# Optimization experiments

Measured on AMD Instinct MI355X. Metric: run time of the kernel, lower is better.

## Reference

```python
import jax, jax.numpy as jnp
import numpy as np

N, E, IN, H, OUT = 100000, 600000, 128, 128, 64
BN_EPS = 1e-5


def setup_inputs() -> dict:
    key = jax.random.key(0)
    ks = jax.random.split(key, 8)
    def lin(k, i, o):
        return jax.random.normal(k, (i, o), jnp.float32) / np.float32(np.sqrt(i))
    return {
        "x": jax.random.normal(ks[0], (N, IN), jnp.float32),
        "edge_index": jax.random.randint(ks[1], (2, E), 0, N, dtype=jnp.int64),
        "W1": lin(ks[2], IN, H), "b1": jnp.zeros((H,), jnp.float32),
        "gamma": jnp.ones((H,), jnp.float32), "beta": jnp.zeros((H,), jnp.float32),
        "W2": lin(ks[3], H, H), "b2": jnp.zeros((H,), jnp.float32),
        "Wm1": lin(ks[4], H, H), "bm1": jnp.zeros((H,), jnp.float32),
        "Wm2": lin(ks[5], H, OUT), "bm2": jnp.zeros((OUT,), jnp.float32),
    }


def reference(x, edge_index, W1, b1, gamma, beta, W2, b2, Wm1, bm1, Wm2, bm2):
    # GINConv: h = MLP((1 + eps) * x + sum_{j in N(i)} x_j), eps = 0 (train_eps=False)
    src = edge_index[0]
    dst = edge_index[1]  # PyG aggregates messages at edge_index[1]
    agg = jax.ops.segment_sum(x[src], dst, num_segments=x.shape[0])  # [N, IN]
    h = agg + x
    # inner MLP: Linear -> BatchNorm (batch stats) -> ReLU -> Linear
    h = h @ W1 + b1
    mean = jnp.mean(h, axis=0)
    var = jnp.var(h, axis=0)
    h = (h - mean) * jax.lax.rsqrt(var + BN_EPS) * gamma + beta
    h = jax.nn.relu(h)
    h = h @ W2 + b2
    h = jax.nn.relu(h)  # .relu() after conv
    # output MLP (norm=None, dropout=0.5 -> identity at inference): Linear -> ReLU -> Linear
    h = jax.nn.relu(h @ Wm1 + bm1)
    return h @ Wm2 + bm2
```

## Files before the change

kernel.cpp:

```cpp
#include <hip/hip_runtime.h>
#include <hip/hip_bf16.h>
#include <stdint.h>

#define NNODES 100000
#define NEDGES 600000
#define SCAN_CHUNK 1024
#define SCAN_NB 98

typedef __attribute__((ext_vector_type(8))) short bf16x8;
typedef __attribute__((ext_vector_type(4))) float f32x4;

__device__ inline float b2f(short b) {
    union { unsigned u; float f; } v;
    v.u = ((unsigned)(unsigned short)b) << 16;
    return v.f;
}
__device__ inline short f2b(float f) {
    union { float f; unsigned u; } v;
    v.f = f;
    unsigned r = (v.u + 0x7FFFu + ((v.u >> 16) & 1u)) >> 16;
    return (short)r;
}
__device__ inline int swz(int row, int kbyte) {
    return (row * 256 + kbyte) ^ ((row & 7) << 4);
}
#define MFMA16(a, b, c) __builtin_amdgcn_mfma_f32_16x16x32_bf16(a, b, c, 0, 0, 0)

__global__ __launch_bounds__(256) void k_prep(const float* __restrict__ x,
                                              const float* __restrict__ W1,
                                              const float* __restrict__ W2,
                                              const float* __restrict__ Wm1,
                                              const float* __restrict__ Wm2,
                                              short* __restrict__ xb, short* __restrict__ Wt,
                                              int* __restrict__ pos, float* __restrict__ stats) {
    int i = blockIdx.x * 256 + threadIdx.x;
    if (i < (NNODES + 1) * 16) {
        bf16x8 o = (bf16x8){0, 0, 0, 0, 0, 0, 0, 0};
        if (i < NNODES * 16) {
            const float4* p = (const float4*)(x + (size_t)i * 8);
            float4 a = p[0], b = p[1];
            o[0] = f2b(a.x); o[1] = f2b(a.y); o[2] = f2b(a.z); o[3] = f2b(a.w);
            o[4] = f2b(b.x); o[5] = f2b(b.y); o[6] = f2b(b.z); o[7] = f2b(b.w);
        }
        *(bf16x8*)(xb + (size_t)i * 8) = o;
    }
    if (i < NNODES) pos[i] = 0;
    if (i < 57344) {
        float v;
        int c, k, base, ncb;
        if (i < 16384) {
            c = i >> 7; k = i & 127; v = W1[k * 128 + c]; base = 0; ncb = 8;
        } else if (i < 32768) {
            int j = i - 16384; c = j >> 7; k = j & 127; v = W2[k * 128 + c]; base = 16384; ncb = 8;
        } else if (i < 49152) {
            int j = i - 32768; c = j >> 7; k = j & 127; v = Wm1[k * 128 + c]; base = 32768; ncb = 8;
        } else {
            int j = i - 49152; c = j >> 7; k = j & 127; v = Wm2[k * 64 + c]; base = 49152; ncb = 4;
        }
        int kb = k >> 5, hi = (k >> 3) & 3, jj = k & 7;
        int cb = c >> 4, lr = c & 15;
        int lane = hi * 16 + lr;
        int dst = base + (((kb * ncb) + cb) * 64 + lane) * 8 + jj;
        Wt[dst] = f2b(v);
    }
    if (i < 256) stats[i] = 0.0f;
}


__global__ __launch_bounds__(256) void k_hist(const int* __restrict__ ei, int* __restrict__ cnt) {
    int e = blockIdx.x * 256 + threadIdx.x;
    if (e < NEDGES) atomicAdd(&cnt[ei[NEDGES + e]], 1);
}

__global__ __launch_bounds__(256) void k_scan1(const int* __restrict__ cnt, int* __restrict__ bsums) {
    __shared__ int sd[256];
    int b = blockIdx.x, t = threadIdx.x;
    int base = b * SCAN_CHUNK + t * 4;
    int s = 0;
#pragma unroll
    for (int i = 0; i < 4; ++i) {
        int idx = base + i;
        if (idx < NNODES) s += cnt[idx];
    }
    sd[t] = s;
    __syncthreads();
    for (int off = 128; off > 0; off >>= 1) {
        if (t < off) sd[t] += sd[t + off];
        __syncthreads();
    }
    if (t == 0) bsums[b] = sd[0];
}

__global__ __launch_bounds__(64) void k_scan2(int* __restrict__ bsums, int* __restrict__ rowptr) {
    if (threadIdx.x == 0 && blockIdx.x == 0) {
        int run = 0;
        for (int b = 0; b < SCAN_NB; ++b) {
            int v = bsums[b];
            bsums[b] = run;
            run += v;
        }
        rowptr[NNODES] = run;
    }
}

__global__ __launch_bounds__(256) void k_scan3(const int* __restrict__ cnt,
                                               const int* __restrict__ bsums,
                                               int* __restrict__ rowptr, int* __restrict__ pos) {
    __shared__ int sd[256];
    int b = blockIdx.x, t = threadIdx.x;
    int base = b * SCAN_CHUNK + t * 4;
    int v[4];
    int s = 0;
#pragma unroll
    for (int i = 0; i < 4; ++i) {
        int idx = base + i;
        v[i] = (idx < NNODES) ? cnt[idx] : 0;
        s += v[i];
    }
    sd[t] = s;
    __syncthreads();
    for (int off = 1; off < 256; off <<= 1) {
        int val = (t >= off) ? sd[t - off] : 0;
        __syncthreads();
        sd[t] += val;
        __syncthreads();
    }
    int run = sd[t] - s + bsums[b];
#pragma unroll
    for (int i = 0; i < 4; ++i) {
        int idx = base + i;
        if (idx < NNODES) {
            rowptr[idx] = run;
            pos[idx] = run;
            run += v[i];
        }
    }
}

__global__ __launch_bounds__(256) void k_fill(const int* __restrict__ ei, int* __restrict__ pos,
                                              int* __restrict__ elist) {
    int e = blockIdx.x * 256 + threadIdx.x;
    if (e >= NEDGES) return;
    int src = ei[e];
    int dst = ei[NEDGES + e];
    int p = atomicAdd(&pos[dst], 1);
    elist[p] = src;
}

__global__ __launch_bounds__(256) void k_agg(const short* __restrict__ xb,
                                             const int* __restrict__ rowptr,
                                             const int* __restrict__ elist,
                                             short* __restrict__ bufb) {
    int t = threadIdx.x;
    int w = t >> 6, lane = t & 63;
    int node = blockIdx.x * 4 + w;
    if (node >= NNODES) return;
    int beg = rowptr[node];
    int end = rowptr[node + 1];
    int deg = end - beg;
    int total = deg + 1;
    int sub = lane & 31, half = lane >> 5;
    const uint2* xr = (const uint2*)xb;

    float acc0 = 0.f, acc1 = 0.f, acc2 = 0.f, acc3 = 0.f;

    for (int base = 0; base < total; base += 64) {
        int j = base + lane;
        int ej = NNODES;
        if (j < total) ej = (j == 0) ? node : elist[beg + j - 1];
        int cnt = min(64, total - base);
        int pairs = (cnt + 1) >> 1;
        for (int i = 0; i < pairs; i += 4) {
            int j0 = 2 * i + half;
            int r0 = __shfl(ej, j0);
            int r1 = __shfl(ej, j0 + 2);
            int r2 = __shfl(ej, j0 + 4);
            int r3 = __shfl(ej, j0 + 6);
            uint2 v0 = xr[(size_t)r0 * 32 + sub];
            uint2 v1 = xr[(size_t)r1 * 32 + sub];
            uint2 v2 = xr[(size_t)r2 * 32 + sub];
            uint2 v3 = xr[(size_t)r3 * 32 + sub];
            acc0 += b2f((short)(v0.x & 0xFFFF)) + b2f((short)(v1.x & 0xFFFF)) +
                    b2f((short)(v2.x & 0xFFFF)) + b2f((short)(v3.x & 0xFFFF));
            acc1 += b2f((short)(v0.x >> 16)) + b2f((short)(v1.x >> 16)) +
                    b2f((short)(v2.x >> 16)) + b2f((short)(v3.x >> 16));
            acc2 += b2f((short)(v0.y & 0xFFFF)) + b2f((short)(v1.y & 0xFFFF)) +
                    b2f((short)(v2.y & 0xFFFF)) + b2f((short)(v3.y & 0xFFFF));
            acc3 += b2f((short)(v0.y >> 16)) + b2f((short)(v1.y >> 16)) +
                    b2f((short)(v2.y >> 16)) + b2f((short)(v3.y >> 16));
        }
    }
    acc0 += __shfl_xor(acc0, 32);
    acc1 += __shfl_xor(acc1, 32);
    acc2 += __shfl_xor(acc2, 32);
    acc3 += __shfl_xor(acc3, 32);
    if (half == 0) {
        uint2 o;
        o.x = ((uint32_t)(unsigned short)f2b(acc1) << 16) | (uint32_t)(unsigned short)f2b(acc0);
        o.y = ((uint32_t)(unsigned short)f2b(acc3) << 16) | (uint32_t)(unsigned short)f2b(acc2);
        ((uint2*)bufb)[(size_t)node * 32 + sub] = o;
    }
}

__global__ __launch_bounds__(256) void k_stats(const short* __restrict__ bufb,
                                               const short* __restrict__ W1pk,
                                               float* __restrict__ stats) {
    __shared__ float Sred[2][4][128];
    int t = threadIdx.x, w = t >> 6, l = t & 63;
    int r0 = blockIdx.x * 128;
    int row0 = (w & 1) * 64, col0 = (w >> 1) * 64;

    f32x4 acc[4][4];
#pragma unroll
    for (int r = 0; r < 4; ++r)
#pragma unroll
        for (int c = 0; c < 4; ++c) acc[r][c] = (f32x4){0.f, 0.f, 0.f, 0.f};

#pragma unroll
    for (int kb = 0; kb < 4; ++kb) {
        bf16x8 af[4], bw[4];
#pragma unroll
        for (int r = 0; r < 4; ++r)
            af[r] = *(const bf16x8*)(bufb + (size_t)(r0 + row0 + r * 16 + (l & 15)) * 128 +
                                     kb * 32 + (l >> 4) * 8);
#pragma unroll
        for (int c = 0; c < 4; ++c)
            bw[c] = *(const bf16x8*)(W1pk + ((kb * 8 + (w >> 1) * 4 + c) * 64 + l) * 8);
#pragma unroll
        for (int r = 0; r < 4; ++r)
#pragma unroll
            for (int c = 0; c < 4; ++c) acc[r][c] = MFMA16(af[r], bw[c], acc[r][c]);
    }

    float s[4], q[4];
#pragma unroll
    for (int c = 0; c < 4; ++c) { s[c] = 0.f; q[c] = 0.f; }
#pragma unroll
    for (int c = 0; c < 4; ++c)
#pragma unroll
        for (int r = 0; r < 4; ++r)
#pragma unroll
            for (int rr = 0; rr < 4; ++rr) {
                int grow = r0 + row0 + r * 16 + (l >> 4) * 4 + rr;
                if (grow < NNODES) {
                    float v = acc[r][c][rr];
                    s[c] += v;
                    q[c] += v * v;
                }
            }
#pragma unroll
    for (int c = 0; c < 4; ++c) {
        s[c] += __shfl_xor(s[c], 16); s[c] += __shfl_xor(s[c], 32);
        q[c] += __shfl_xor(q[c], 16); q[c] += __shfl_xor(q[c], 32);
    }
    if (l < 16) {
#pragma unroll
        for (int c = 0; c < 4; ++c) {
            Sred[0][w][col0 + c * 16 + l] = s[c];
            Sred[1][w][col0 + c * 16 + l] = q[c];
        }
    }
    __syncthreads();
    if (t < 128) {
        int wb = (t < 64) ? 0 : 2;
        atomicAdd(stats + t, Sred[0][wb][t] + Sred[0][wb + 1][t]);
        atomicAdd(stats + 128 + t, Sred[1][wb][t] + Sred[1][wb + 1][t]);
    }
}

__global__ __launch_bounds__(256) void k_mlp(const short* __restrict__ bufb,
                                             const float* __restrict__ stats,
                                             const float* __restrict__ gamma,
                                             const float* __restrict__ beta,
                                             const short* __restrict__ Wt,
                                             const float* __restrict__ b2,
                                             const float* __restrict__ bm1,
                                             const float* __restrict__ bm2,
                                             float* __restrict__ out) {
    __shared__ __align__(16) short act[128 * 128];
    __shared__ float scale[128], shift[128];

    int t = threadIdx.x, w = t >> 6, l = t & 63;
    int r0 = blockIdx.x * 128;
    const short* W1pk = Wt;
    const short* W2pk = Wt + 16384;
    const short* Wm1pk = Wt + 32768;
    const short* Wm2pk = Wt + 49152;

    if (t < 128) {
        float mean = stats[t] * (1.0f / NNODES);
        float var = stats[128 + t] * (1.0f / NNODES) - mean * mean;
        var = fmaxf(var, 0.0f);
        float inv = rsqrtf(var + 1e-5f);
        float sc = gamma[t] * inv;
        scale[t] = sc;
        shift[t] = beta[t] - mean * sc;
    }
    __syncthreads();

    int row0 = (w & 1) * 64, col0 = (w >> 1) * 64;
    f32x4 acc[4][4];

#pragma unroll
    for (int r = 0; r < 4; ++r)
#pragma unroll
        for (int c = 0; c < 4; ++c) acc[r][c] = (f32x4){0.f, 0.f, 0.f, 0.f};
#pragma unroll
    for (int kb = 0; kb < 4; ++kb) {
        bf16x8 af[4], bw[4];
#pragma unroll
        for (int r = 0; r < 4; ++r)
            af[r] = *(const bf16x8*)(bufb + (size_t)(r0 + row0 + r * 16 + (l & 15)) * 128 +
                                     kb * 32 + (l >> 4) * 8);
#pragma unroll
        for (int c = 0; c < 4; ++c)
            bw[c] = *(const bf16x8*)(W1pk + ((kb * 8 + (w >> 1) * 4 + c) * 64 + l) * 8);
#pragma unroll
        for (int r = 0; r < 4; ++r)
#pragma unroll
            for (int c = 0; c < 4; ++c) acc[r][c] = MFMA16(af[r], bw[c], acc[r][c]);
    }
#pragma unroll
    for (int c = 0; c < 4; ++c) {
        int col = col0 + c * 16 + (l & 15);
        float sc_ = scale[col], sh_ = shift[col];
#pragma unroll
        for (int r = 0; r < 4; ++r)
#pragma unroll
            for (int rr = 0; rr < 4; ++rr) {
                int row = row0 + r * 16 + (l >> 4) * 4 + rr;
                *(short*)((char*)act + swz(row, col * 2)) =
                    f2b(fmaxf(acc[r][c][rr] * sc_ + sh_, 0.f));
            }
    }
    __syncthreads();

#pragma unroll
    for (int r = 0; r < 4; ++r)
#pragma unroll
        for (int c = 0; c < 4; ++c) acc[r][c] = (f32x4){0.f, 0.f, 0.f, 0.f};
#pragma unroll
    for (int kb = 0; kb < 4; ++kb) {
        int kbyte = kb * 64 + (l >> 4) * 16;
        bf16x8 af[4], bw[4];
#pragma unroll
        for (int r = 0; r < 4; ++r)
            af[r] = *(const bf16x8*)((char*)act + swz(row0 + r * 16 + (l & 15), kbyte));
#pragma unroll
        for (int c = 0; c < 4; ++c)
            bw[c] = *(const bf16x8*)(W2pk + ((kb * 8 + (w >> 1) * 4 + c) * 64 + l) * 8);
#pragma unroll
        for (int r = 0; r < 4; ++r)
#pragma unroll
            for (int c = 0; c < 4; ++c) acc[r][c] = MFMA16(af[r], bw[c], acc[r][c]);
    }
    __syncthreads();
#pragma unroll
    for (int c = 0; c < 4; ++c) {
        int col = col0 + c * 16 + (l & 15);
        float bias = b2[col];
#pragma unroll
        for (int r = 0; r < 4; ++r)
#pragma unroll
            for (int rr = 0; rr < 4; ++rr) {
                int row = row0 + r * 16 + (l >> 4) * 4 + rr;
                *(short*)((char*)act + swz(row, col * 2)) = f2b(fmaxf(acc[r][c][rr] + bias, 0.f));
            }
    }
    __syncthreads();

#pragma unroll
    for (int r = 0; r < 4; ++r)
#pragma unroll
        for (int c = 0; c < 4; ++c) acc[r][c] = (f32x4){0.f, 0.f, 0.f, 0.f};
#pragma unroll
    for (int kb = 0; kb < 4; ++kb) {
        int kbyte = kb * 64 + (l >> 4) * 16;
        bf16x8 af[4], bw[4];
#pragma unroll
        for (int r = 0; r < 4; ++r)
            af[r] = *(const bf16x8*)((char*)act + swz(row0 + r * 16 + (l & 15), kbyte));
#pragma unroll
        for (int c = 0; c < 4; ++c)
            bw[c] = *(const bf16x8*)(Wm1pk + ((kb * 8 + (w >> 1) * 4 + c) * 64 + l) * 8);
#pragma unroll
        for (int r = 0; r < 4; ++r)
#pragma unroll
            for (int c = 0; c < 4; ++c) acc[r][c] = MFMA16(af[r], bw[c], acc[r][c]);
    }
    __syncthreads();
#pragma unroll
    for (int c = 0; c < 4; ++c) {
        int col = col0 + c * 16 + (l & 15);
        float bias = bm1[col];
#pragma unroll
        for (int r = 0; r < 4; ++r)
#pragma unroll
            for (int rr = 0; rr < 4; ++rr) {
                int row = row0 + r * 16 + (l >> 4) * 4 + rr;
                *(short*)((char*)act + swz(row, col * 2)) = f2b(fmaxf(acc[r][c][rr] + bias, 0.f));
            }
    }
    __syncthreads();

    int row0q = w * 32;
    f32x4 a2[2][4];
#pragma unroll
    for (int r = 0; r < 2; ++r)
#pragma unroll
        for (int c = 0; c < 4; ++c) a2[r][c] = (f32x4){0.f, 0.f, 0.f, 0.f};
#pragma unroll
    for (int kb = 0; kb < 4; ++kb) {
        int kbyte = kb * 64 + (l >> 4) * 16;
        bf16x8 af[2], bw[4];
#pragma unroll
        for (int r = 0; r < 2; ++r)
            af[r] = *(const bf16x8*)((char*)act + swz(row0q + r * 16 + (l & 15), kbyte));
#pragma unroll
        for (int c = 0; c < 4; ++c)
            bw[c] = *(const bf16x8*)(Wm2pk + ((kb * 4 + c) * 64 + l) * 8);
#pragma unroll
        for (int r = 0; r < 2; ++r)
#pragma unroll
            for (int c = 0; c < 4; ++c) a2[r][c] = MFMA16(af[r], bw[c], a2[r][c]);
    }
#pragma unroll
    for (int c = 0; c < 4; ++c) {
        float bias = bm2[c * 16 + (l & 15)];
#pragma unroll
        for (int r = 0; r < 2; ++r)
#pragma unroll
            for (int rr = 0; rr < 4; ++rr) {
                int grow = r0 + row0q + r * 16 + (l >> 4) * 4 + rr;
                if (grow < NNODES)
                    out[(size_t)grow * 64 + c * 16 + (l & 15)] = a2[r][c][rr] + bias;
            }
    }
}

extern "C" void kernel_launch(void* const* d_in, const int* in_sizes, int n_in,
                              void* d_out, int out_size, void* d_ws, size_t ws_size,
                              hipStream_t stream) {
    const float* x     = (const float*)d_in[0];
    const int*   ei    = (const int*)d_in[1];
    const float* W1    = (const float*)d_in[2];
    const float* gamma = (const float*)d_in[4];
    const float* beta  = (const float*)d_in[5];
    const float* W2    = (const float*)d_in[6];
    const float* b2    = (const float*)d_in[7];
    const float* Wm1   = (const float*)d_in[8];
    const float* bm1   = (const float*)d_in[9];
    const float* Wm2   = (const float*)d_in[10];
    const float* bm2   = (const float*)d_in[11];
    float* out = (float*)d_out;

    char* ws = (char*)d_ws;
    short* xb    = (short*)ws;
    short* bufb  = xb + (size_t)(NNODES + 1) * 128;
    short* Wt    = bufb + (size_t)(NNODES + 128) * 128;
    float* stats = (float*)(Wt + 57344);
    int* rowptr  = (int*)(stats + 256);
    int* pos     = rowptr + (NNODES + 1);
    int* elist   = pos + NNODES;
    int* bsums   = elist + NEDGES;

    int gE = (NEDGES + 255) / 256;
    int gPrep = ((NNODES + 1) * 16 + 255) / 256;

    k_prep<<<gPrep, 256, 0, stream>>>(x, W1, W2, Wm1, Wm2, xb, Wt, pos, stats);
    k_hist<<<gE, 256, 0, stream>>>(ei, pos);
    k_scan1<<<SCAN_NB, 256, 0, stream>>>(pos, bsums);
    k_scan2<<<1, 64, 0, stream>>>(bsums, rowptr);
    k_scan3<<<SCAN_NB, 256, 0, stream>>>(pos, bsums, rowptr, pos);
    k_fill<<<gE, 256, 0, stream>>>(ei, pos, elist);
    k_agg<<<(NNODES + 3) / 4, 256, 0, stream>>>(xb, rowptr, elist, bufb);

    int nblk = (NNODES + 127) / 128;
    k_stats<<<nblk, 256, 0, stream>>>(bufb, Wt, stats);
    k_mlp<<<nblk, 256, 0, stream>>>(bufb, stats, gamma, beta, Wt, b2, bm1, bm2, out);
}
```

Measured before the change: 180.1 us.

## Restructure MLP kernel to single-wave 64-row blocks without barriers

The fused MLP kernel now runs one 64-thread wave per 64-row tile instead of four waves per 128-row tile. Each wave computes all 128 output columns in two passes, so every __syncthreads between layers is gone. A-fragments for all K blocks are held in registers, and biases are staged in shared memory. The kernel also raises wave priority with s_setprio around the MFMA loops and cuts per-block LDS, which should allow more blocks per CU. In exchange, each block loads the weights twice as often relative to rows computed, and register pressure rises from holding 16 A fragments.

```diff
diff --git a/kernel.cpp b/kernel.cpp
--- a/kernel.cpp
+++ b/kernel.cpp
@@ -268,172 +268,198 @@
     }
 }
 
-__global__ __launch_bounds__(256) void k_mlp(const short* __restrict__ bufb,
-                                             const float* __restrict__ stats,
-                                             const float* __restrict__ gamma,
-                                             const float* __restrict__ beta,
-                                             const short* __restrict__ Wt,
-                                             const float* __restrict__ b2,
-                                             const float* __restrict__ bm1,
-                                             const float* __restrict__ bm2,
-                                             float* __restrict__ out) {
-    __shared__ __align__(16) short act[128 * 128];
-    __shared__ float scale[128], shift[128];
-
-    int t = threadIdx.x, w = t >> 6, l = t & 63;
-    int r0 = blockIdx.x * 128;
+__global__ __launch_bounds__(64) void k_mlp(const short* __restrict__ bufb,
+                                            const float* __restrict__ stats,
+                                            const float* __restrict__ gamma,
+                                            const float* __restrict__ beta,
+                                            const short* __restrict__ Wt,
+                                            const float* __restrict__ b2,
+                                            const float* __restrict__ bm1,
+                                            const float* __restrict__ bm2,
+                                            float* __restrict__ out) {
+    __shared__ __align__(16) short act[64 * 128];
+    __shared__ float scale[128], shift[128], b2s[128], bm1s[128], bm2s[64];
+
+    int l = threadIdx.x;
+    int lr = l & 15, hi = l >> 4;
+    size_t r0w = (size_t)blockIdx.x * 64;
     const short* W1pk = Wt;
     const short* W2pk = Wt + 16384;
     const short* Wm1pk = Wt + 32768;
     const short* Wm2pk = Wt + 49152;
 
-    if (t < 128) {
-        float mean = stats[t] * (1.0f / NNODES);
-        float var = stats[128 + t] * (1.0f / NNODES) - mean * mean;
+#pragma unroll
+    for (int i = 0; i < 2; ++i) {
+        int idx = l + i * 64;
+        float mean = stats[idx] * (1.0f / NNODES);
+        float var = stats[128 + idx] * (1.0f / NNODES) - mean * mean;
         var = fmaxf(var, 0.0f);
         float inv = rsqrtf(var + 1e-5f);
-        float sc = gamma[t] * inv;
-        scale[t] = sc;
-        shift[t] = beta[t] - mean * sc;
-    }
+        float sc = gamma[idx] * inv;
+        scale[idx] = sc;
+        shift[idx] = beta[idx] - mean * sc;
+        b2s[idx] = b2[idx];
+        bm1s[idx] = bm1[idx];
+    }
+    bm2s[l] = bm2[l];
     __syncthreads();
 
-    int row0 = (w & 1) * 64, col0 = (w >> 1) * 64;
+    bf16x8 af[4][4];
     f32x4 acc[4][4];
 
 #pragma unroll
+    for (int kb = 0; kb < 4; ++kb)
+#pragma unroll
+        for (int r = 0; r < 4; ++r)
+            af[kb][r] = *(const bf16x8*)(bufb + (r0w + r * 16 + lr) * 128 + kb * 32 + hi * 8);
+
+#pragma unroll
+    for (int p = 0; p < 2; ++p) {
+#pragma unroll
+        for (int r = 0; r < 4; ++r)
+#pragma unroll
+            for (int c = 0; c < 4; ++c) acc[r][c] = (f32x4){0.f, 0.f, 0.f, 0.f};
+        __builtin_amdgcn_s_setprio(1);
+#pragma unroll
+        for (int kb = 0; kb < 4; ++kb) {
+            bf16x8 bw[4];
+#pragma unroll
+            for (int c = 0; c < 4; ++c)
+                bw[c] = *(const bf16x8*)(W1pk + ((kb * 8 + p * 4 + c) * 64 + l) * 8);
+#pragma unroll
+            for (int r = 0; r < 4; ++r)
+#pragma unroll
+                for (int c = 0; c < 4; ++c) acc[r][c] = MFMA16(af[kb][r], bw[c], acc[r][c]);
+        }
+        __builtin_amdgcn_s_setprio(0);
+#pragma unroll
+        for (int c = 0; c < 4; ++c) {
+            int col = p * 64 + c * 16 + lr;
+            float sc_ = scale[col], sh_ = shift[col];
+#pragma unroll
+            for (int r = 0; r < 4; ++r)
+#pragma unroll
+                for (int rr = 0; rr < 4; ++rr) {
+                    int row = r * 16 + hi * 4 + rr;
+                    *(short*)((char*)act + swz(row, col * 2)) =
+                        f2b(fmaxf(acc[r][c][rr] * sc_ + sh_, 0.f));
+                }
+        }
+    }
+
+#pragma unroll
+    for (int kb = 0; kb < 4; ++kb)
+#pragma unroll
+        for (int r = 0; r < 4; ++r)
+            af[kb][r] = *(const bf16x8*)((char*)act + swz(r * 16 + lr, kb * 64 + hi * 16));
+
+#pragma unroll
+    for (int p = 0; p < 2; ++p) {
+#pragma unroll
+        for (int r = 0; r < 4; ++r)
+#pragma unroll
+            for (int c = 0; c < 4; ++c) acc[r][c] = (f32x4){0.f, 0.f, 0.f, 0.f};
+        __builtin_amdgcn_s_setprio(1);
+#pragma unroll
+        for (int kb = 0; kb < 4; ++kb) {
+            bf16x8 bw[4];
+#pragma unroll
+            for (int c = 0; c < 4; ++c)
+                bw[c] = *(const bf16x8*)(W2pk + ((kb * 8 + p * 4 + c) * 64 + l) * 8);
+#pragma unroll
+            for (int r = 0; r < 4; ++r)
+#pragma unroll
+                for (int c = 0; c < 4; ++c) acc[r][c] = MFMA16(af[kb][r], bw[c], acc[r][c]);
+        }
+        __builtin_amdgcn_s_setprio(0);
+#pragma unroll
+        for (int c = 0; c < 4; ++c) {
+            int col = p * 64 + c * 16 + lr;
+            float bias = b2s[col];
+#pragma unroll
+            for (int r = 0; r < 4; ++r)
+#pragma unroll
+                for (int rr = 0; rr < 4; ++rr) {
+                    int row = r * 16 + hi * 4 + rr;
+                    *(short*)((char*)act + swz(row, col * 2)) =
+                        f2b(fmaxf(acc[r][c][rr] + bias, 0.f));
+                }
+        }
+    }
+
+#pragma unroll
+    for (int kb = 0; kb < 4; ++kb)
+#pragma unroll
+        for (int r = 0; r < 4; ++r)
+            af[kb][r] = *(const bf16x8*)((char*)act + swz(r * 16 + lr, kb * 64 + hi * 16));
+
+#pragma unroll
+    for (int p = 0; p < 2; ++p) {
+#pragma unroll
+        for (int r = 0; r < 4; ++r)
+#pragma unroll
+            for (int c = 0; c < 4; ++c) acc[r][c] = (f32x4){0.f, 0.f, 0.f, 0.f};
+        __builtin_amdgcn_s_setprio(1);
+#pragma unroll
+        for (int kb = 0; kb < 4; ++kb) {
+            bf16x8 bw[4];
+#pragma unroll
+            for (int c = 0; c < 4; ++c)
+                bw[c] = *(const bf16x8*)(Wm1pk + ((kb * 8 + p * 4 + c) * 64 + l) * 8);
+#pragma unroll
+            for (int r = 0; r < 4; ++r)
+#pragma unroll
+                for (int c = 0; c < 4; ++c) acc[r][c] = MFMA16(af[kb][r], bw[c], acc[r][c]);
+        }
+        __builtin_amdgcn_s_setprio(0);
+#pragma unroll
+        for (int c = 0; c < 4; ++c) {
+            int col = p * 64 + c * 16 + lr;
+            float bias = bm1s[col];
+#pragma unroll
+            for (int r = 0; r < 4; ++r)
+#pragma unroll
+                for (int rr = 0; rr < 4; ++rr) {
+                    int row = r * 16 + hi * 4 + rr;
+                    *(short*)((char*)act + swz(row, col * 2)) =
+                        f2b(fmaxf(acc[r][c][rr] + bias, 0.f));
+                }
+        }
+    }
+
+#pragma unroll
+    for (int kb = 0; kb < 4; ++kb)
+#pragma unroll
+        for (int r = 0; r < 4; ++r)
+            af[kb][r] = *(const bf16x8*)((char*)act + swz(r * 16 + lr, kb * 64 + hi * 16));
+
+#pragma unroll
     for (int r = 0; r < 4; ++r)
 #pragma unroll
         for (int c = 0; c < 4; ++c) acc[r][c] = (f32x4){0.f, 0.f, 0.f, 0.f};
+    __builtin_amdgcn_s_setprio(1);
 #pragma unroll
     for (int kb = 0; kb < 4; ++kb) {
-        bf16x8 af[4], bw[4];
-#pragma unroll
-        for (int r = 0; r < 4; ++r)
-            af[r] = *(const bf16x8*)(bufb + (size_t)(r0 + row0 + r * 16 + (l & 15)) * 128 +
-                                     kb * 32 + (l >> 4) * 8);
-#pragma unroll
-        for (int c = 0; c < 4; ++c)
-            bw[c] = *(const bf16x8*)(W1pk + ((kb * 8 + (w >> 1) * 4 + c) * 64 + l) * 8);
-#pragma unroll
-        for (int r = 0; r < 4; ++r)
-#pragma unroll
-            for (int c = 0; c < 4; ++c) acc[r][c] = MFMA16(af[r], bw[c], acc[r][c]);
-    }
-#pragma unroll
-    for (int c = 0; c < 4; ++c) {
-        int col = col0 + c * 16 + (l & 15);
-        float sc_ = scale[col], sh_ = shift[col];
-#pragma unroll
-        for (int r = 0; r < 4; ++r)
-#pragma unroll
-            for (int rr = 0; rr < 4; ++rr) {
-                int row = row0 + r * 16 + (l >> 4) * 4 + rr;
-                *(short*)((char*)act + swz(row, col * 2)) =
-                    f2b(fmaxf(acc[r][c][rr] * sc_ + sh_, 0.f));
-            }
-    }
-    __syncthreads();
-
-#pragma unroll
-    for (int r = 0; r < 4; ++r)
-#pragma unroll
-        for (int c = 0; c < 4; ++c) acc[r][c] = (f32x4){0.f, 0.f, 0.f, 0.f};
-#pragma unroll
-    for (int kb = 0; kb < 4; ++kb) {
-        int kbyte = kb * 64 + (l >> 4) * 16;
-        bf16x8 af[4], bw[4];
-#pragma unroll
-        for (int r = 0; r < 4; ++r)
-            af[r] = *(const bf16x8*)((char*)act + swz(row0 + r * 16 + (l & 15), kbyte));
-#pragma unroll
-        for (int c = 0; c < 4; ++c)
-            bw[c] = *(const bf16x8*)(W2pk + ((kb * 8 + (w >> 1) * 4 + c) * 64 + l) * 8);
-#pragma unroll
-        for (int r = 0; r < 4; ++r)
-#pragma unroll
-            for (int c = 0; c < 4; ++c) acc[r][c] = MFMA16(af[r], bw[c], acc[r][c]);
-    }
-    __syncthreads();
-#pragma unroll
-    for (int c = 0; c < 4; ++c) {
-        int col = col0 + c * 16 + (l & 15);
-        float bias = b2[col];
-#pragma unroll
-        for (int r = 0; r < 4; ++r)
-#pragma unroll
-            for (int rr = 0; rr < 4; ++rr) {
-                int row = row0 + r * 16 + (l >> 4) * 4 + rr;
-                *(short*)((char*)act + swz(row, col * 2)) = f2b(fmaxf(acc[r][c][rr] + bias, 0.f));
-            }
-    }
-    __syncthreads();
-
-#pragma unroll
-    for (int r = 0; r < 4; ++r)
-#pragma unroll
-        for (int c = 0; c < 4; ++c) acc[r][c] = (f32x4){0.f, 0.f, 0.f, 0.f};
-#pragma unroll
-    for (int kb = 0; kb < 4; ++kb) {
-        int kbyte = kb * 64 + (l >> 4) * 16;
-        bf16x8 af[4], bw[4];
-#pragma unroll
-        for (int r = 0; r < 4; ++r)
-            af[r] = *(const bf16x8*)((char*)act + swz(row0 + r * 16 + (l & 15), kbyte));
-#pragma unroll
-        for (int c = 0; c < 4; ++c)
-            bw[c] = *(const bf16x8*)(Wm1pk + ((kb * 8 + (w >> 1) * 4 + c) * 64 + l) * 8);
-#pragma unroll
-        for (int r = 0; r < 4; ++r)
-#pragma unroll
-            for (int c = 0; c < 4; ++c) acc[r][c] = MFMA16(af[r], bw[c], acc[r][c]);
-    }
-    __syncthreads();
-#pragma unroll
-    for (int c = 0; c < 4; ++c) {
-        int col = col0 + c * 16 + (l & 15);
-        float bias = bm1[col];
-#pragma unroll
-        for (int r = 0; r < 4; ++r)
-#pragma unroll
-            for (int rr = 0; rr < 4; ++rr) {
-                int row = row0 + r * 16 + (l >> 4) * 4 + rr;
-                *(short*)((char*)act + swz(row, col * 2)) = f2b(fmaxf(acc[r][c][rr] + bias, 0.f));
-            }
-    }
-    __syncthreads();
-
-    int row0q = w * 32;
-    f32x4 a2[2][4];
-#pragma unroll
-    for (int r = 0; r < 2; ++r)
-#pragma unroll
-        for (int c = 0; c < 4; ++c) a2[r][c] = (f32x4){0.f, 0.f, 0.f, 0.f};
-#pragma unroll
-    for (int kb = 0; kb < 4; ++kb) {
-        int kbyte = kb * 64 + (l >> 4) * 16;
-        bf16x8 af[2], bw[4];
-#pragma unroll
-        for (int r = 0; r < 2; ++r)
-            af[r] = *(const bf16x8*)((char*)act + swz(row0q + r * 16 + (l & 15), kbyte));
+        bf16x8 bw[4];
 #pragma unroll
         for (int c = 0; c < 4; ++c)
             bw[c] = *(const bf16x8*)(Wm2pk + ((kb * 4 + c) * 64 + l) * 8);
 #pragma unroll
-        for (int r = 0; r < 2; ++r)
-#pragma unroll
-            for (int c = 0; c < 4; ++c) a2[r][c] = MFMA16(af[r], bw[c], a2[r][c]);
-    }
+        for (int r = 0; r < 4; ++r)
+#pragma unroll
+            for (int c = 0; c < 4; ++c) acc[r][c] = MFMA16(af[kb][r], bw[c], acc[r][c]);
+    }
+    __builtin_amdgcn_s_setprio(0);
 #pragma unroll
     for (int c = 0; c < 4; ++c) {
-        float bias = bm2[c * 16 + (l & 15)];
-#pragma unroll
-        for (int r = 0; r < 2; ++r)
+        float bias = bm2s[c * 16 + lr];
+#pragma unroll
+        for (int r = 0; r < 4; ++r)
 #pragma unroll
             for (int rr = 0; rr < 4; ++rr) {
-                int grow = r0 + row0q + r * 16 + (l >> 4) * 4 + rr;
+                size_t grow = r0w + r * 16 + hi * 4 + rr;
                 if (grow < NNODES)
-                    out[(size_t)grow * 64 + c * 16 + (l & 15)] = a2[r][c][rr] + bias;
+                    out[grow * 64 + c * 16 + lr] = acc[r][c][rr] + bias;
             }
     }
 }
@@ -475,7 +501,8 @@
     k_fill<<<gE, 256, 0, stream>>>(ei, pos, elist);
     k_agg<<<(NNODES + 3) / 4, 256, 0, stream>>>(xb, rowptr, elist, bufb);
 
-    int nblk = (NNODES + 127) / 128;
-    k_stats<<<nblk, 256, 0, stream>>>(bufb, Wt, stats);
-    k_mlp<<<nblk, 256, 0, stream>>>(bufb, stats, gamma, beta, Wt, b2, bm1, bm2, out);
-}
+    int nblkS = (NNODES + 127) / 128;
+    k_stats<<<nblkS, 256, 0, stream>>>(bufb, Wt, stats);
+    int nblkM = (NNODES + 63) / 64;
+    k_mlp<<<nblkM, 64, 0, stream>>>(bufb, stats, gamma, beta, Wt, b2, bm1, bm2, out);
+}
```

After: 183.5 us. Within noise of the previous version (+1.9%).

## Keep MLP chain in registers via transposed MFMA and shuffle redistribution; single-block scan

Applied to the files above, without the earlier changes.

The MLP kernel is restructured so each wave owns 16 nodes and computes transposed products (W^T·h), holding activations in registers. Between layers the outputs are repacked to bf16 and redistributed across lanes with shuffles, which removes the shared-memory activation tile and its barriers. Weights are repacked ct-major to match this access order, and launch bounds ask for higher occupancy. The three-kernel scan is replaced by a single 1024-thread block, which cuts launches but serialises the scan onto one CU with strided per-thread loops.

```diff
diff --git a/kernel.cpp b/kernel.cpp
--- a/kernel.cpp
+++ b/kernel.cpp
@@ -4,11 +4,10 @@
 
 #define NNODES 100000
 #define NEDGES 600000
-#define SCAN_CHUNK 1024
-#define SCAN_NB 98
 
 typedef __attribute__((ext_vector_type(8))) short bf16x8;
 typedef __attribute__((ext_vector_type(4))) float f32x4;
+typedef __attribute__((ext_vector_type(4))) unsigned int u32x4;
 
 __device__ inline float b2f(short b) {
     union { unsigned u; float f; } v;
@@ -21,8 +20,8 @@
     unsigned r = (v.u + 0x7FFFu + ((v.u >> 16) & 1u)) >> 16;
     return (short)r;
 }
-__device__ inline int swz(int row, int kbyte) {
-    return (row * 256 + kbyte) ^ ((row & 7) << 4);
+__device__ inline unsigned packbf(float lo, float hi) {
+    return ((unsigned)(unsigned short)f2b(hi) << 16) | (unsigned)(unsigned short)f2b(lo);
 }
 #define MFMA16(a, b, c) __builtin_amdgcn_mfma_f32_16x16x32_bf16(a, b, c, 0, 0, 0)
 
@@ -46,22 +45,21 @@
     }
     if (i < NNODES) pos[i] = 0;
     if (i < 57344) {
-        float v;
-        int c, k, base, ncb;
-        if (i < 16384) {
-            c = i >> 7; k = i & 127; v = W1[k * 128 + c]; base = 0; ncb = 8;
-        } else if (i < 32768) {
-            int j = i - 16384; c = j >> 7; k = j & 127; v = W2[k * 128 + c]; base = 16384; ncb = 8;
-        } else if (i < 49152) {
-            int j = i - 32768; c = j >> 7; k = j & 127; v = Wm1[k * 128 + c]; base = 32768; ncb = 8;
-        } else {
-            int j = i - 49152; c = j >> 7; k = j & 127; v = Wm2[k * 64 + c]; base = 49152; ncb = 4;
-        }
-        int kb = k >> 5, hi = (k >> 3) & 3, jj = k & 7;
-        int cb = c >> 4, lr = c & 15;
-        int lane = hi * 16 + lr;
-        int dst = base + (((kb * ncb) + cb) * 64 + lane) * 8 + jj;
-        Wt[dst] = f2b(v);
+        int jj, lane, kt, ct;
+        const float* W;
+        int ldw, off;
+        if (i < 16384) { off = i; W = W1; ldw = 128; }
+        else if (i < 32768) { off = i - 16384; W = W2; ldw = 128; }
+        else if (i < 49152) { off = i - 32768; W = Wm1; ldw = 128; }
+        else { off = i - 49152; W = Wm2; ldw = 64; }
+        jj = off & 7;
+        lane = (off >> 3) & 63;
+        kt = (off >> 9) & 3;
+        ct = (off >> 11) & 7;
+        int lr = lane & 15, hi = lane >> 4;
+        int c = ct * 16 + lr;
+        int k = kt * 32 + hi * 8 + jj;
+        Wt[i] = f2b(W[k * ldw + c]);
     }
     if (i < 256) stats[i] = 0.0f;
 }
@@ -72,69 +70,35 @@
     if (e < NEDGES) atomicAdd(&cnt[ei[NEDGES + e]], 1);
 }
 
-__global__ __launch_bounds__(256) void k_scan1(const int* __restrict__ cnt, int* __restrict__ bsums) {
-    __shared__ int sd[256];
-    int b = blockIdx.x, t = threadIdx.x;
-    int base = b * SCAN_CHUNK + t * 4;
+__global__ __launch_bounds__(1024) void k_scan(const int* __restrict__ cnt,
+                                               int* __restrict__ rowptr, int* __restrict__ pos) {
+    __shared__ int sd[1024];
+    int t = threadIdx.x;
+    int base = t * 98;
     int s = 0;
-#pragma unroll
-    for (int i = 0; i < 4; ++i) {
+    for (int i = 0; i < 98; ++i) {
         int idx = base + i;
         if (idx < NNODES) s += cnt[idx];
     }
     sd[t] = s;
     __syncthreads();
-    for (int off = 128; off > 0; off >>= 1) {
-        if (t < off) sd[t] += sd[t + off];
+    for (int off = 1; off < 1024; off <<= 1) {
+        int v = (t >= off) ? sd[t - off] : 0;
         __syncthreads();
-    }
-    if (t == 0) bsums[b] = sd[0];
-}
-
-__global__ __launch_bounds__(64) void k_scan2(int* __restrict__ bsums, int* __restrict__ rowptr) {
-    if (threadIdx.x == 0 && blockIdx.x == 0) {
-        int run = 0;
-        for (int b = 0; b < SCAN_NB; ++b) {
-            int v = bsums[b];
-            bsums[b] = run;
-            run += v;
-        }
-        rowptr[NNODES] = run;
-    }
-}
-
-__global__ __launch_bounds__(256) void k_scan3(const int* __restrict__ cnt,
-                                               const int* __restrict__ bsums,
-                                               int* __restrict__ rowptr, int* __restrict__ pos) {
-    __shared__ int sd[256];
-    int b = blockIdx.x, t = threadIdx.x;
-    int base = b * SCAN_CHUNK + t * 4;
-    int v[4];
-    int s = 0;
-#pragma unroll
-    for (int i = 0; i < 4; ++i) {
-        int idx = base + i;
-        v[i] = (idx < NNODES) ? cnt[idx] : 0;
-        s += v[i];
-    }
-    sd[t] = s;
-    __syncthreads();
-    for (int off = 1; off < 256; off <<= 1) {
-        int val = (t >= off) ? sd[t - off] : 0;
+        sd[t] += v;
         __syncthreads();
-        sd[t] += val;
-        __syncthreads();
-    }
-    int run = sd[t] - s + bsums[b];
-#pragma unroll
-    for (int i = 0; i < 4; ++i) {
+    }
+    int run = sd[t] - s;
+    for (int i = 0; i < 98; ++i) {
         int idx = base + i;
         if (idx < NNODES) {
+            int v = cnt[idx];
             rowptr[idx] = run;
             pos[idx] = run;
-            run += v[i];
-        }
-    }
+            run += v;
+        }
+    }
+    if (t == 1023) rowptr[NNODES] = run;
 }
 
 __global__ __launch_bounds__(256) void k_fill(const int* __restrict__ ei, int* __restrict__ pos,
@@ -225,7 +189,7 @@
                                      kb * 32 + (l >> 4) * 8);
 #pragma unroll
         for (int c = 0; c < 4; ++c)
-            bw[c] = *(const bf16x8*)(W1pk + ((kb * 8 + (w >> 1) * 4 + c) * 64 + l) * 8);
+            bw[c] = *(const bf16x8*)(W1pk + ((((w >> 1) * 4 + c) * 4 + kb) * 64 + l) * 8);
 #pragma unroll
         for (int r = 0; r < 4; ++r)
 #pragma unroll
@@ -268,20 +232,20 @@
     }
 }
 
-__global__ __launch_bounds__(256) void k_mlp(const short* __restrict__ bufb,
-                                             const float* __restrict__ stats,
-                                             const float* __restrict__ gamma,
-                                             const float* __restrict__ beta,
-                                             const short* __restrict__ Wt,
-                                             const float* __restrict__ b2,
-                                             const float* __restrict__ bm1,
-                                             const float* __restrict__ bm2,
-                                             float* __restrict__ out) {
-    __shared__ __align__(16) short act[128 * 128];
-    __shared__ float scale[128], shift[128];
+__global__ __launch_bounds__(256, 4) void k_mlp(const short* __restrict__ bufb,
+                                                const float* __restrict__ stats,
+                                                const float* __restrict__ gamma,
+                                                const float* __restrict__ beta,
+                                                const short* __restrict__ Wt,
+                                                const float* __restrict__ b2,
+                                                const float* __restrict__ bm1,
+                                                const float* __restrict__ bm2,
+                                                float* __restrict__ out) {
+    __shared__ float scale[128], shift[128], b2s[128], bm1s[128], bm2s[64];
 
     int t = threadIdx.x, w = t >> 6, l = t & 63;
-    int r0 = blockIdx.x * 128;
+    int lr = l & 15, hi = l >> 4;
+    size_t node0 = (size_t)blockIdx.x * 64 + w * 16;
     const short* W1pk = Wt;
     const short* W2pk = Wt + 16384;
     const short* Wm1pk = Wt + 32768;
@@ -295,146 +259,99 @@
         float sc = gamma[t] * inv;
         scale[t] = sc;
         shift[t] = beta[t] - mean * sc;
-    }
+        b2s[t] = b2[t];
+        bm1s[t] = bm1[t];
+    }
+    if (t < 64) bm2s[t] = bm2[t];
     __syncthreads();
 
-    int row0 = (w & 1) * 64, col0 = (w >> 1) * 64;
-    f32x4 acc[4][4];
-
-#pragma unroll
-    for (int r = 0; r < 4; ++r)
-#pragma unroll
-        for (int c = 0; c < 4; ++c) acc[r][c] = (f32x4){0.f, 0.f, 0.f, 0.f};
-#pragma unroll
-    for (int kb = 0; kb < 4; ++kb) {
-        bf16x8 af[4], bw[4];
-#pragma unroll
-        for (int r = 0; r < 4; ++r)
-            af[r] = *(const bf16x8*)(bufb + (size_t)(r0 + row0 + r * 16 + (l & 15)) * 128 +
-                                     kb * 32 + (l >> 4) * 8);
-#pragma unroll
-        for (int c = 0; c < 4; ++c)
-            bw[c] = *(const bf16x8*)(W1pk + ((kb * 8 + (w >> 1) * 4 + c) * 64 + l) * 8);
-#pragma unroll
-        for (int r = 0; r < 4; ++r)
-#pragma unroll
-            for (int c = 0; c < 4; ++c) acc[r][c] = MFMA16(af[r], bw[c], acc[r][c]);
-    }
-#pragma unroll
-    for (int c = 0; c < 4; ++c) {
-        int col = col0 + c * 16 + (l & 15);
-        float sc_ = scale[col], sh_ = shift[col];
-#pragma unroll
-        for (int r = 0; r < 4; ++r)
-#pragma unroll
-            for (int rr = 0; rr < 4; ++rr) {
-                int row = row0 + r * 16 + (l >> 4) * 4 + rr;
-                *(short*)((char*)act + swz(row, col * 2)) =
-                    f2b(fmaxf(acc[r][c][rr] * sc_ + sh_, 0.f));
-            }
-    }
-    __syncthreads();
-
-#pragma unroll
-    for (int r = 0; r < 4; ++r)
-#pragma unroll
-        for (int c = 0; c < 4; ++c) acc[r][c] = (f32x4){0.f, 0.f, 0.f, 0.f};
-#pragma unroll
-    for (int kb = 0; kb < 4; ++kb) {
-        int kbyte = kb * 64 + (l >> 4) * 16;
-        bf16x8 af[4], bw[4];
-#pragma unroll
-        for (int r = 0; r < 4; ++r)
-            af[r] = *(const bf16x8*)((char*)act + swz(row0 + r * 16 + (l & 15), kbyte));
-#pragma unroll
-        for (int c = 0; c < 4; ++c)
-            bw[c] = *(const bf16x8*)(W2pk + ((kb * 8 + (w >> 1) * 4 + c) * 64 + l) * 8);
-#pragma unroll
-        for (int r = 0; r < 4; ++r)
-#pragma unroll
-            for (int c = 0; c < 4; ++c) acc[r][c] = MFMA16(af[r], bw[c], acc[r][c]);
-    }
-    __syncthreads();
-#pragma unroll
-    for (int c = 0; c < 4; ++c) {
-        int col = col0 + c * 16 + (l & 15);
-        float bias = b2[col];
-#pragma unroll
-        for (int r = 0; r < 4; ++r)
-#pragma unroll
-            for (int rr = 0; rr < 4; ++rr) {
-                int row = row0 + r * 16 + (l >> 4) * 4 + rr;
-                *(short*)((char*)act + swz(row, col * 2)) = f2b(fmaxf(acc[r][c][rr] + bias, 0.f));
-            }
-    }
-    __syncthreads();
-
-#pragma unroll
-    for (int r = 0; r < 4; ++r)
-#pragma unroll
-        for (int c = 0; c < 4; ++c) acc[r][c] = (f32x4){0.f, 0.f, 0.f, 0.f};
-#pragma unroll
-    for (int kb = 0; kb < 4; ++kb) {
-        int kbyte = kb * 64 + (l >> 4) * 16;
-        bf16x8 af[4], bw[4];
-#pragma unroll
-        for (int r = 0; r < 4; ++r)
-            af[r] = *(const bf16x8*)((char*)act + swz(row0 + r * 16 + (l & 15), kbyte));
-#pragma unroll
-        for (int c = 0; c < 4; ++c)
-            bw[c] = *(const bf16x8*)(Wm1pk + ((kb * 8 + (w >> 1) * 4 + c) * 64 + l) * 8);
-#pragma unroll
-        for (int r = 0; r < 4; ++r)
-#pragma unroll
-            for (int c = 0; c < 4; ++c) acc[r][c] = MFMA16(af[r], bw[c], acc[r][c]);
-    }
-    __syncthreads();
-#pragma unroll
-    for (int c = 0; c < 4; ++c) {
-        int col = col0 + c * 16 + (l & 15);
-        float bias = bm1[col];
-#pragma unroll
-        for (int r = 0; r < 4; ++r)
-#pragma unroll
-            for (int rr = 0; rr < 4; ++rr) {
-                int row = row0 + r * 16 + (l >> 4) * 4 + rr;
-                *(short*)((char*)act + swz(row, col * 2)) = f2b(fmaxf(acc[r][c][rr] + bias, 0.f));
-            }
-    }
-    __syncthreads();
-
-    int row0q = w * 32;
-    f32x4 a2[2][4];
-#pragma unroll
-    for (int r = 0; r < 2; ++r)
-#pragma unroll
-        for (int c = 0; c < 4; ++c) a2[r][c] = (f32x4){0.f, 0.f, 0.f, 0.f};
-#pragma unroll
-    for (int kb = 0; kb < 4; ++kb) {
-        int kbyte = kb * 64 + (l >> 4) * 16;
-        bf16x8 af[2], bw[4];
-#pragma unroll
-        for (int r = 0; r < 2; ++r)
-            af[r] = *(const bf16x8*)((char*)act + swz(row0q + r * 16 + (l & 15), kbyte));
-#pragma unroll
-        for (int c = 0; c < 4; ++c)
-            bw[c] = *(const bf16x8*)(Wm2pk + ((kb * 4 + c) * 64 + l) * 8);
-#pragma unroll
-        for (int r = 0; r < 2; ++r)
-#pragma unroll
-            for (int c = 0; c < 4; ++c) a2[r][c] = MFMA16(af[r], bw[c], a2[r][c]);
-    }
-#pragma unroll
-    for (int c = 0; c < 4; ++c) {
-        float bias = bm2[c * 16 + (l & 15)];
-#pragma unroll
-        for (int r = 0; r < 2; ++r)
-#pragma unroll
-            for (int rr = 0; rr < 4; ++rr) {
-                int grow = r0 + row0q + r * 16 + (l >> 4) * 4 + rr;
-                if (grow < NNODES)
-                    out[(size_t)grow * 64 + c * 16 + (l & 15)] = a2[r][c][rr] + bias;
-            }
+    bf16x8 bv[4];
+#pragma unroll
+    for (int kt = 0; kt < 4; ++kt)
+        bv[kt] = *(const bf16x8*)(bufb + (node0 + lr) * 128 + kt * 32 + hi * 8);
+
+    unsigned pw[8][2];
+
+#pragma unroll
+    for (int ct = 0; ct < 8; ++ct) {
+        f32x4 a = (f32x4){0.f, 0.f, 0.f, 0.f};
+#pragma unroll
+        for (int kt = 0; kt < 4; ++kt)
+            a = MFMA16(*(const bf16x8*)(W1pk + ((ct * 4 + kt) * 64 + l) * 8), bv[kt], a);
+        int c0 = ct * 16 + hi * 4;
+        float4 sc4 = *(const float4*)&scale[c0];
+        float4 sh4 = *(const float4*)&shift[c0];
+        float v0 = fmaxf(a[0] * sc4.x + sh4.x, 0.f);
+        float v1 = fmaxf(a[1] * sc4.y + sh4.y, 0.f);
+        float v2 = fmaxf(a[2] * sc4.z + sh4.z, 0.f);
+        float v3 = fmaxf(a[3] * sc4.w + sh4.w, 0.f);
+        pw[ct][0] = packbf(v0, v1);
+        pw[ct][1] = packbf(v2, v3);
+    }
+
+#define REDIST()                                                                        \
+    {                                                                                   \
+        int h2 = hi >> 1, h1 = hi & 1;                                                  \
+        _Pragma("unroll") for (int kt = 0; kt < 4; ++kt) {                              \
+            unsigned nw[4];                                                             \
+            _Pragma("unroll") for (int jp = 0; jp < 4; ++jp) {                          \
+                int srcl = (2 * h1 + (jp >> 1)) * 16 + lr;                              \
+                unsigned ve = (unsigned)__shfl((int)pw[2 * kt][jp & 1], srcl);          \
+                unsigned vo = (unsigned)__shfl((int)pw[2 * kt + 1][jp & 1], srcl);      \
+                nw[jp] = h2 ? vo : ve;                                                  \
+            }                                                                           \
+            u32x4 uq = (u32x4){nw[0], nw[1], nw[2], nw[3]};                             \
+            bv[kt] = __builtin_bit_cast(bf16x8, uq);                                    \
+        }                                                                               \
+    }
+    REDIST();
+
+#pragma unroll
+    for (int ct = 0; ct < 8; ++ct) {
+        f32x4 a = (f32x4){0.f, 0.f, 0.f, 0.f};
+#pragma unroll
+        for (int kt = 0; kt < 4; ++kt)
+            a = MFMA16(*(const bf16x8*)(W2pk + ((ct * 4 + kt) * 64 + l) * 8), bv[kt], a);
+        int c0 = ct * 16 + hi * 4;
+        float4 bb = *(const float4*)&b2s[c0];
+        float v0 = fmaxf(a[0] + bb.x, 0.f);
+        float v1 = fmaxf(a[1] + bb.y, 0.f);
+        float v2 = fmaxf(a[2] + bb.z, 0.f);
+        float v3 = fmaxf(a[3] + bb.w, 0.f);
+        pw[ct][0] = packbf(v0, v1);
+        pw[ct][1] = packbf(v2, v3);
+    }
+    REDIST();
+
+#pragma unroll
+    for (int ct = 0; ct < 8; ++ct) {
+        f32x4 a = (f32x4){0.f, 0.f, 0.f, 0.f};
+#pragma unroll
+        for (int kt = 0; kt < 4; ++kt)
+            a = MFMA16(*(const bf16x8*)(Wm1pk + ((ct * 4 + kt) * 64 + l) * 8), bv[kt], a);
+        int c0 = ct * 16 + hi * 4;
+        float4 bb = *(const float4*)&bm1s[c0];
+        float v0 = fmaxf(a[0] + bb.x, 0.f);
+        float v1 = fmaxf(a[1] + bb.y, 0.f);
+        float v2 = fmaxf(a[2] + bb.z, 0.f);
+        float v3 = fmaxf(a[3] + bb.w, 0.f);
+        pw[ct][0] = packbf(v0, v1);
+        pw[ct][1] = packbf(v2, v3);
+    }
+    REDIST();
+
+#pragma unroll
+    for (int ct = 0; ct < 4; ++ct) {
+        f32x4 a = (f32x4){0.f, 0.f, 0.f, 0.f};
+#pragma unroll
+        for (int kt = 0; kt < 4; ++kt)
+            a = MFMA16(bv[kt], *(const bf16x8*)(Wm2pk + ((ct * 4 + kt) * 64 + l) * 8), a);
+        float bias = bm2s[ct * 16 + lr];
+#pragma unroll
+        for (int rr = 0; rr < 4; ++rr) {
+            size_t grow = node0 + hi * 4 + rr;
+            if (grow < NNODES) out[grow * 64 + ct * 16 + lr] = a[rr] + bias;
+        }
     }
 }
 
@@ -462,20 +379,18 @@
     int* rowptr  = (int*)(stats + 256);
     int* pos     = rowptr + (NNODES + 1);
     int* elist   = pos + NNODES;
-    int* bsums   = elist + NEDGES;
 
     int gE = (NEDGES + 255) / 256;
     int gPrep = ((NNODES + 1) * 16 + 255) / 256;
 
     k_prep<<<gPrep, 256, 0, stream>>>(x, W1, W2, Wm1, Wm2, xb, Wt, pos, stats);
     k_hist<<<gE, 256, 0, stream>>>(ei, pos);
-    k_scan1<<<SCAN_NB, 256, 0, stream>>>(pos, bsums);
-    k_scan2<<<1, 64, 0, stream>>>(bsums, rowptr);
-    k_scan3<<<SCAN_NB, 256, 0, stream>>>(pos, bsums, rowptr, pos);
+    k_scan<<<1, 1024, 0, stream>>>(pos, rowptr, pos);
     k_fill<<<gE, 256, 0, stream>>>(ei, pos, elist);
     k_agg<<<(NNODES + 3) / 4, 256, 0, stream>>>(xb, rowptr, elist, bufb);
 
-    int nblk = (NNODES + 127) / 128;
-    k_stats<<<nblk, 256, 0, stream>>>(bufb, Wt, stats);
-    k_mlp<<<nblk, 256, 0, stream>>>(bufb, stats, gamma, beta, Wt, b2, bm1, bm2, out);
-}
+    int nblkS = (NNODES + 127) / 128;
+    k_stats<<<nblkS, 256, 0, stream>>>(bufb, Wt, stats);
+    int nblkM = (NNODES + 63) / 64;
+    k_mlp<<<nblkM, 256, 0, stream>>>(bufb, stats, gamma, beta, Wt, b2, bm1, bm2, out);
+}
```

After: 435.3 us. 2.42x slower.
